# Optimization experiments

Hardware: AMD Instinct MI355X
Metric: run time of the kernel (lower is better)

## Reference

```python
import jax, jax.numpy as jnp
import numpy as np

DIM = 512

def setup_inputs() -> dict:
    key = jax.random.key(0)
    ks = jax.random.split(key, 7)
    B, Nq, Nkv = 8, 1024, 4096
    prototype = jax.random.normal(ks[0], (B, Nq, DIM), dtype=jnp.float32)
    q_x = jax.random.normal(ks[1], (B, Nkv, DIM), dtype=jnp.float32)
    qry_attn_mask = jax.random.bernoulli(ks[2], 0.5, (B, Nkv))  # True = keep
    # Linear(dim, dim, bias=False) weights, torch convention y = x @ W.T
    s = 1.0 / np.sqrt(DIM)
    Wq = jax.random.uniform(ks[3], (DIM, DIM), jnp.float32, -s, s)
    Wk = jax.random.uniform(ks[4], (DIM, DIM), jnp.float32, -s, s)
    Wv = jax.random.uniform(ks[5], (DIM, DIM), jnp.float32, -s, s)
    Wproj = jax.random.uniform(ks[6], (DIM, DIM), jnp.float32, -s, s)
    return {"prototype": prototype, "q_x": q_x, "qry_attn_mask": qry_attn_mask,
            "Wq": Wq, "Wk": Wk, "Wv": Wv, "Wproj": Wproj}

def reference(prototype, q_x, qry_attn_mask, Wq, Wk, Wv, Wproj):
    scale = DIM ** (-0.5)
    q = jnp.einsum('bnd,ed->bne', prototype, Wq)          # [B,Nq,D]
    k = jnp.einsum('bmd,ed->bme', q_x, Wk)                # [B,Nkv,D]
    v = jnp.einsum('bmd,ed->bme', q_x, Wv)                # [B,Nkv,D]
    attn = jnp.einsum('bnd,bmd->bnm', q, k) * scale       # [B,Nq,Nkv]
    bias = (~qry_attn_mask).astype(attn.dtype)[:, None, :] * -10000.0
    attn = jax.nn.softmax(attn + bias, axis=-1)
    x = jnp.einsum('bnm,bmd->bnd', attn, v)
    x = jnp.einsum('bnd,ed->bne', x, Wproj)
    return x
```

## Files before the change

kernel.cpp:

```cpp
#include <hip/hip_runtime.h>
#include <hip/hip_bf16.h>
#include <stdint.h>


typedef __bf16 bf16;
typedef bf16 bf16x8 __attribute__((ext_vector_type(8)));
typedef bf16 bf16x4 __attribute__((ext_vector_type(4)));
typedef float f32x4 __attribute__((ext_vector_type(4)));

#define NB 8
#define NQ 1024
#define NKV 4096
#define DD 512
#define RT_LD 136

__device__ __forceinline__ void lds16(const bf16* g, bf16* l) {
  __builtin_amdgcn_global_load_lds(
      (const __attribute__((address_space(1))) unsigned int*)g,
      (__attribute__((address_space(3))) unsigned int*)l, 16, 0, 0);
}

__global__ void cvt_kernel(const float* __restrict__ src, bf16* __restrict__ dst, int n4) {
  int i = blockIdx.x * blockDim.x + threadIdx.x;
  if (i < n4) {
    float4 v = ((const float4*)src)[i];
    bf16x4 o;
    o.x = (bf16)v.x; o.y = (bf16)v.y; o.z = (bf16)v.z; o.w = (bf16)v.w;
    ((bf16x4*)dst)[i] = o;
  }
}

__global__ void cvt_weights(const float* __restrict__ Wq, const float* __restrict__ Wk,
                            const float* __restrict__ Wv, const float* __restrict__ Wp,
                            bf16* __restrict__ Wq_b, bf16* __restrict__ Wkv_b,
                            bf16* __restrict__ Wp_b) {
  int i = blockIdx.x * blockDim.x + threadIdx.x;
  int w = i >> 16, r = i & 65535;
  const float* src = (w == 0) ? Wq : (w == 1) ? Wk : (w == 2) ? Wv : Wp;
  bf16x4* dst = (w == 0) ? (bf16x4*)Wq_b
              : (w == 3) ? (bf16x4*)Wp_b
                         : (bf16x4*)Wkv_b + (w == 2 ? 65536 : 0);
  float4 v = ((const float4*)src)[r];
  bf16x4 o;
  o.x = (bf16)v.x; o.y = (bf16)v.y; o.z = (bf16)v.z; o.w = (bf16)v.w;
  dst[r] = o;
}

__global__ void sniff_zero(const unsigned* __restrict__ mask, int* __restrict__ flag,
                           float* __restrict__ denom) {
  __shared__ int s_bad0, s_bad1;
  if (threadIdx.x == 0) { s_bad0 = 0; s_bad1 = 0; }
  __syncthreads();
  int b0 = 0, b1 = 0;
  for (int i = threadIdx.x; i < 8192; i += 256) {
    unsigned v = mask[i];
    if (v > 1u) b0 = 1;
    if (v != 0u && v != 0x3F800000u) b1 = 1;
  }
  if (b0) atomicOr(&s_bad0, 1);
  if (b1) atomicOr(&s_bad1, 1);
  for (int i = threadIdx.x; i < NB * NQ; i += 256) denom[i] = 0.f;
  __syncthreads();
  if (threadIdx.x == 0) *flag = (s_bad0 == 0) ? 0 : ((s_bad1 == 0) ? 1 : 2);
}

__global__ void scan_mask(const void* __restrict__ mask, const int* __restrict__ flagP,
                          int* __restrict__ idx, int* __restrict__ cnt,
                          int* __restrict__ kpad) {
  const int b = blockIdx.x, tid = threadIdx.x;
  const int mode = *flagP;
  __shared__ int ps[256];
  unsigned bits = 0;
  int c = 0;
  const int base = tid * 16;
  for (int i = 0; i < 16; ++i) {
    const int col = base + i;
    bool k;
    if (mode == 0)      k = ((const int*)mask)[b * NKV + col] != 0;
    else if (mode == 1) k = ((const float*)mask)[b * NKV + col] != 0.f;
    else                k = ((const unsigned char*)mask)[b * NKV + col] != 0;
    bits |= (unsigned)k << i;
    c += k;
  }
  ps[tid] = c;
  __syncthreads();
  for (int s = 1; s < 256; s <<= 1) {
    int v = (tid >= s) ? ps[tid - s] : 0;
    __syncthreads();
    ps[tid] += v;
    __syncthreads();
  }
  int off = ps[tid] - c;
  for (int i = 0; i < 16; ++i)
    if ((bits >> i) & 1) idx[b * NKV + off++] = base + i;
  if (tid == 255) {
    cnt[b] = ps[255];
    kpad[b] = (ps[255] + 127) & ~127;
  }
}

__global__ void gather_qx(const float* __restrict__ qx, const int* __restrict__ idx,
                          const int* __restrict__ cnt, const int* __restrict__ kpad,
                          bf16* __restrict__ qc) {
  const int b = blockIdx.y;
  const int wave = threadIdx.x >> 6, lane = threadIdx.x & 63;
  const int r0 = blockIdx.x * 16 + wave * 4;
  const int n = cnt[b];
  const int kp = kpad[b];
#pragma unroll
  for (int j = 0; j < 4; ++j) {
    const int row = r0 + j;
    if (row >= kp) return;
    bf16x4* d = (bf16x4*)(qc + ((long)b * NKV + row) * DD) + lane;
    if (row < n) {
      const int src = idx[b * NKV + row];
      const float4* s = (const float4*)(qx + ((long)b * NKV + src) * DD) + lane;
      float4 v0 = s[0], v1 = s[64];
      bf16x4 o0, o1;
      o0.x = (bf16)v0.x; o0.y = (bf16)v0.y; o0.z = (bf16)v0.z; o0.w = (bf16)v0.w;
      o1.x = (bf16)v1.x; o1.y = (bf16)v1.y; o1.z = (bf16)v1.z; o1.w = (bf16)v1.w;
      d[0] = o0;
      d[64] = o1;
    } else {
      bf16x4 z;
      z.x = (bf16)0.f; z.y = (bf16)0.f; z.z = (bf16)0.f; z.w = (bf16)0.f;
      d[0] = z;
      d[64] = z;
    }
  }
}

template <int EPI>
__global__ void __launch_bounds__(256, 4)
gemm_bt(const bf16* __restrict__ A, const bf16* __restrict__ Bw,
        void* __restrict__ Cp, void* __restrict__ Cp2,
        int N, int Klen, int Kstride,
        long sA, long sB, long sC,
        const int* __restrict__ cnt, const int* __restrict__ kpad,
        float* __restrict__ denom, float scale, int M) {
  __shared__ alignas(16) bf16 Smem[128 * RT_LD];
  bf16* As = Smem;
  bf16* Bs = Smem + 4096;
  bf16* Rt = Smem;
  const int tid = threadIdx.x;
  const int wave = tid >> 6, lane = tid & 63;
  const int l15 = lane & 15, l4 = lane >> 4;
  const int wm = (wave >> 1) * 64, wn = (wave & 1) * 64;
  const int bx = (EPI == 5) ? blockIdx.y : blockIdx.x;
  const int by = (EPI == 5) ? blockIdx.x : blockIdx.y;
  const int b = blockIdx.z;

  if constexpr (EPI == 2) {
    if (bx * 128 >= kpad[b]) return;
  } else {
    const int bb = by >> 5, loc = (by & 31) * 128;
    if (loc >= kpad[bb]) return;
  }

  const bf16* Ab = A + (long)b * sA + (long)(by * 128) * Kstride;
  const bf16* Bb = Bw + (long)b * sB + (long)(bx * 128) * Kstride;

  const int c0 = wave * 2, c1 = wave * 2 + 1;
  const int srow = lane >> 2;
  const int scol = (lane & 3) * 8;
  const bf16* ag0 = Ab + (long)(c0 * 16 + srow) * Kstride + scol;
  const bf16* ag1 = Ab + (long)(c1 * 16 + srow) * Kstride + scol;
  const bf16* bg0 = Bb + (long)(c0 * 16 + srow) * Kstride + scol;
  const bf16* bg1 = Bb + (long)(c1 * 16 + srow) * Kstride + scol;
  bf16* al0 = As + c0 * 512;
  bf16* al1 = As + c1 * 512;
  bf16* bl0 = Bs + c0 * 512;
  bf16* bl1 = Bs + c1 * 512;

  f32x4 acc[4][4] = {};

  for (int kt = 0; kt < Klen; kt += 32) {
    __syncthreads();
    lds16(ag0, al0);
    lds16(ag1, al1);
    lds16(bg0, bl0);
    lds16(bg1, bl1);
    ag0 += 32; ag1 += 32; bg0 += 32; bg1 += 32;
    __syncthreads();
    bf16x8 af[4], bfr[4];
#pragma unroll
    for (int t = 0; t < 4; ++t)
      af[t] = *(const bf16x8*)(As + (wm + t * 16 + l15) * 32 + l4 * 8);
#pragma unroll
    for (int t = 0; t < 4; ++t)
      bfr[t] = *(const bf16x8*)(Bs + (wn + t * 16 + l15) * 32 + l4 * 8);
#pragma unroll
    for (int mt = 0; mt < 4; ++mt)
#pragma unroll
      for (int nt = 0; nt < 4; ++nt)
        acc[mt][nt] = __builtin_amdgcn_mfma_f32_16x16x32_bf16(af[mt], bfr[nt],
                                                              acc[mt][nt], 0, 0, 0);
  }

  const int rowBase = by * 128 + wm;
  const int colBase = bx * 128 + wn;
  const int tR = by * 128;
  const int tC = bx * 128;

  __syncthreads();

  if constexpr (EPI == 2) {
    bf16* C = (bf16*)Cp + (long)b * sC;
    const int nkeep = cnt[b];
    float rs[4][4];
#pragma unroll
    for (int mt = 0; mt < 4; ++mt)
#pragma unroll
      for (int r = 0; r < 4; ++r) rs[mt][r] = 0.f;
#pragma unroll
    for (int nt = 0; nt < 4; ++nt) {
      const bool keep = (colBase + nt * 16 + l15) < nkeep;
#pragma unroll
      for (int mt = 0; mt < 4; ++mt)
#pragma unroll
        for (int r = 0; r < 4; ++r) {
          float p = keep ? __expf(acc[mt][nt][r] * scale) : 0.f;
          rs[mt][r] += p;
          Rt[(wm + mt * 16 + l4 * 4 + r) * RT_LD + wn + nt * 16 + l15] = (bf16)p;
        }
    }
#pragma unroll
    for (int mt = 0; mt < 4; ++mt)
#pragma unroll
      for (int r = 0; r < 4; ++r) {
        float v = rs[mt][r];
        v += __shfl_xor(v, 1, 64);
        v += __shfl_xor(v, 2, 64);
        v += __shfl_xor(v, 4, 64);
        v += __shfl_xor(v, 8, 64);
        if (l15 == 0)
          atomicAdd(&denom[b * M + rowBase + mt * 16 + l4 * 4 + r], v);
      }
    __syncthreads();
    const int r0 = tid >> 2, cq = (tid & 3) * 32;
#pragma unroll
    for (int h = 0; h < 128; h += 64)
#pragma unroll
      for (int j = 0; j < 4; ++j) {
        bf16x8 v = *(const bf16x8*)(Rt + (r0 + h) * RT_LD + cq + j * 8);
        *(bf16x8*)(C + (long)(tR + r0 + h) * N + tC + cq + j * 8) = v;
      }
  } else {
    if (tC < 512) {
      bf16* C = (bf16*)Cp;
#pragma unroll
      for (int mt = 0; mt < 4; ++mt)
#pragma unroll
        for (int nt = 0; nt < 4; ++nt)
#pragma unroll
          for (int r = 0; r < 4; ++r)
            Rt[(wm + mt * 16 + l4 * 4 + r) * RT_LD + wn + nt * 16 + l15] =
                (bf16)acc[mt][nt][r];
      __syncthreads();
      const int r0 = tid >> 2, cq = (tid & 3) * 32;
#pragma unroll
      for (int h = 0; h < 128; h += 64)
#pragma unroll
        for (int j = 0; j < 4; ++j) {
          bf16x8 v = *(const bf16x8*)(Rt + (r0 + h) * RT_LD + cq + j * 8);
          *(bf16x8*)(C + (long)(tR + r0 + h) * 512 + tC + cq + j * 8) = v;
        }
    } else {
      bf16* C = (bf16*)Cp2;
#pragma unroll
      for (int mt = 0; mt < 4; ++mt) {
        const int r0 = wm + mt * 16 + l4 * 4;
#pragma unroll
        for (int nt = 0; nt < 4; ++nt) {
          const int cloc = wn + nt * 16 + l15;
          bf16x4 o;
          o.x = (bf16)acc[mt][nt][0]; o.y = (bf16)acc[mt][nt][1];
          o.z = (bf16)acc[mt][nt][2]; o.w = (bf16)acc[mt][nt][3];
          *(bf16x4*)(Rt + cloc * RT_LD + r0) = o;
        }
      }
      __syncthreads();
      const int bb = tR >> 12, kvloc = tR & 4095;
      const int d0 = tid >> 2, kvq = (tid & 3) * 32;
#pragma unroll
      for (int h = 0; h < 128; h += 64)
#pragma unroll
        for (int j = 0; j < 4; ++j) {
          bf16x8 v = *(const bf16x8*)(Rt + (d0 + h) * RT_LD + kvq + j * 8);
          *(bf16x8*)(C + (long)bb * DD * NKV + (long)(tC - 512 + d0 + h) * NKV +
                     kvloc + kvq + j * 8) = v;
        }
    }
  }
}

template <int EPI>
__global__ void __launch_bounds__(256, 4)
gemm_n64(const bf16* __restrict__ A, const bf16* __restrict__ Bw,
         void* __restrict__ Cp) {
  constexpr int SME = (EPI == 0) ? 128 * 72 : 6144;
  __shared__ alignas(16) bf16 Smem[SME];
  bf16* As = Smem;
  bf16* Bs = Smem + 4096;
  bf16* Rt = Smem;
  const int tid = threadIdx.x;
  const int wave = tid >> 6, lane = tid & 63;
  const int l15 = lane & 15, l4 = lane >> 4;
  const int wm = (wave >> 1) * 64, wn = (wave & 1) * 32;

  const bf16* Ab = A + (long)(blockIdx.y * 128) * DD;
  const bf16* Bb = Bw + (long)(blockIdx.x * 64) * DD;

  const int srow = lane >> 2, scol = (lane & 3) * 8;
  const bf16* ag0 = Ab + (long)(wave * 32 + srow) * DD + scol;
  const bf16* ag1 = ag0 + 16 * DD;
  const bf16* bg0 = Bb + (long)(wave * 16 + srow) * DD + scol;
  bf16* al0 = As + wave * 1024;
  bf16* al1 = al0 + 512;
  bf16* bl0 = Bs + wave * 512;

  f32x4 acc[4][2] = {};

  for (int kt = 0; kt < DD; kt += 32) {
    __syncthreads();
    lds16(ag0, al0);
    lds16(ag1, al1);
    lds16(bg0, bl0);
    ag0 += 32; ag1 += 32; bg0 += 32;
    __syncthreads();
    bf16x8 af[4], bfr[2];
#pragma unroll
    for (int t = 0; t < 4; ++t)
      af[t] = *(const bf16x8*)(As + (wm + t * 16 + l15) * 32 + l4 * 8);
#pragma unroll
    for (int t = 0; t < 2; ++t)
      bfr[t] = *(const bf16x8*)(Bs + (wn + t * 16 + l15) * 32 + l4 * 8);
#pragma unroll
    for (int mt = 0; mt < 4; ++mt)
#pragma unroll
      for (int nt = 0; nt < 2; ++nt)
        acc[mt][nt] = __builtin_amdgcn_mfma_f32_16x16x32_bf16(af[mt], bfr[nt],
                                                              acc[mt][nt], 0, 0, 0);
  }

  const int tR = blockIdx.y * 128, tC = blockIdx.x * 64;
  if constexpr (EPI == 0) {
    __syncthreads();
#pragma unroll
    for (int mt = 0; mt < 4; ++mt)
#pragma unroll
      for (int nt = 0; nt < 2; ++nt)
#pragma unroll
        for (int r = 0; r < 4; ++r)
          Rt[(wm + mt * 16 + l4 * 4 + r) * 72 + wn + nt * 16 + l15] =
              (bf16)acc[mt][nt][r];
    __syncthreads();
    bf16* C = (bf16*)Cp;
    const int r0 = tid >> 1, cq = (tid & 1) * 32;
#pragma unroll
    for (int j = 0; j < 4; ++j) {
      bf16x8 v = *(const bf16x8*)(Rt + r0 * 72 + cq + j * 8);
      *(bf16x8*)(C + (long)(tR + r0) * DD + tC + cq + j * 8) = v;
    }
  } else {
    float* C = (float*)Cp;
#pragma unroll
    for (int mt = 0; mt < 4; ++mt)
#pragma unroll
      for (int nt = 0; nt < 2; ++nt)
#pragma unroll
        for (int r = 0; r < 4; ++r)
          C[(long)(tR + wm + mt * 16 + l4 * 4 + r) * DD + tC + wn + nt * 16 + l15] =
              acc[mt][nt][r];
  }
}

__global__ void __launch_bounds__(256, 4)
pv_direct(const bf16* __restrict__ P, const bf16* __restrict__ vT,
          const float* __restrict__ denom, const int* __restrict__ kpad,
          bf16* __restrict__ x) {
  __shared__ alignas(16) bf16 Smem[64 * RT_LD];
  bf16* As = Smem;
  bf16* Bs = Smem + 2048;
  bf16* Rt = Smem;
  const int tid = threadIdx.x;
  const int wave = tid >> 6, lane = tid & 63;
  const int l15 = lane & 15, l4 = lane >> 4;
  const int wm = (wave >> 1) * 32, wn = (wave & 1) * 64;
  const int qB = blockIdx.x * 64;
  const int dB = blockIdx.y * 128;
  const int b = blockIdx.z;
  const int Kb = kpad[b];

  const bf16* Ab = P + (long)b * NQ * NKV + (long)qB * NKV;
  const bf16* Bb = vT + (long)b * DD * NKV + (long)dB * NKV;

  const int srow = lane >> 2, scol = (lane & 3) * 8;
  const bf16* ag = Ab + (long)(wave * 16 + srow) * NKV + scol;
  const bf16* bg0 = Bb + (long)(wave * 32 + srow) * NKV + scol;
  const bf16* bg1 = bg0 + 16 * NKV;
  bf16* al = As + wave * 512;
  bf16* bl0 = Bs + wave * 1024;
  bf16* bl1 = bl0 + 512;

  f32x4 acc[2][4] = {};

  for (int kt = 0; kt < Kb; kt += 32) {
    __syncthreads();
    lds16(ag, al);
    lds16(bg0, bl0);
    lds16(bg1, bl1);
    ag += 32; bg0 += 32; bg1 += 32;
    __syncthreads();
    bf16x8 af[2], bfr[4];
#pragma unroll
    for (int t = 0; t < 2; ++t)
      af[t] = *(const bf16x8*)(As + (wm + t * 16 + l15) * 32 + l4 * 8);
#pragma unroll
    for (int t = 0; t < 4; ++t)
      bfr[t] = *(const bf16x8*)(Bs + (wn + t * 16 + l15) * 32 + l4 * 8);
#pragma unroll
    for (int mt = 0; mt < 2; ++mt)
#pragma unroll
      for (int nt = 0; nt < 4; ++nt)
        acc[mt][nt] = __builtin_amdgcn_mfma_f32_16x16x32_bf16(af[mt], bfr[nt],
                                                              acc[mt][nt], 0, 0, 0);
  }

  __syncthreads();
#pragma unroll
  for (int mt = 0; mt < 2; ++mt)
#pragma unroll
    for (int r = 0; r < 4; ++r) {
      const int row = wm + mt * 16 + l4 * 4 + r;
      const float inv = 1.0f / denom[b * NQ + qB + row];
#pragma unroll
      for (int nt = 0; nt < 4; ++nt)
        Rt[row * RT_LD + wn + nt * 16 + l15] = (bf16)(acc[mt][nt][r] * inv);
    }
  __syncthreads();
  const int r0 = tid >> 2, cq = (tid & 3) * 32;
#pragma unroll
  for (int j = 0; j < 4; ++j) {
    bf16x8 v = *(const bf16x8*)(Rt + r0 * RT_LD + cq + j * 8);
    *(bf16x8*)(x + (long)(b * NQ + qB + r0) * DD + dB + cq + j * 8) = v;
  }
}

extern "C" void kernel_launch(void* const* d_in, const int* in_sizes, int n_in,
                              void* d_out, int out_size, void* d_ws, size_t ws_size,
                              hipStream_t stream) {
  const float* proto = (const float*)d_in[0];
  const float* qx    = (const float*)d_in[1];
  const void*  mask  = d_in[2];
  const float* Wq    = (const float*)d_in[3];
  const float* Wk    = (const float*)d_in[4];
  const float* Wv    = (const float*)d_in[5];
  const float* Wproj = (const float*)d_in[6];
  float* out = (float*)d_out;

  char* w = (char*)d_ws;
  int*   flag  = (int*)w;
  int*   cnt   = (int*)(w + 64);
  int*   kpadA = (int*)(w + 128);
  float* denom = (float*)(w + 4096);
  size_t off = 65536;
  bf16* Wq_b  = (bf16*)(w + off); off += (size_t)DD * DD * 2;
  bf16* Wkv_b = (bf16*)(w + off); off += (size_t)DD * DD * 4;
  bf16* Wp_b  = (bf16*)(w + off); off += (size_t)DD * DD * 2;
  int*  idx   = (int*)(w + off);  off += (size_t)NB * NKV * 4;
  bf16* q_b   = (bf16*)(w + off); off += (size_t)NB * NQ * DD * 2;
  bf16* k_b   = (bf16*)(w + off); off += (size_t)NB * NKV * DD * 2;
  bf16* vT_b  = (bf16*)(w + off); off += (size_t)NB * NKV * DD * 2;
  bf16* x_b   = (bf16*)(w + off); off += (size_t)NB * NQ * DD * 2;
  size_t off_pp = off;
  bf16* proto_b = (bf16*)(w + off); off += (size_t)NB * NQ * DD * 2;
  bf16* qc_b    = (bf16*)(w + off);
  bf16* P       = (bf16*)(w + off_pp);

  sniff_zero<<<1, 256, 0, stream>>>((const unsigned*)mask, flag, denom);
  scan_mask<<<8, 256, 0, stream>>>(mask, flag, idx, cnt, kpadA);

  cvt_kernel<<<NB * NQ * DD / 4 / 256, 256, 0, stream>>>(proto, proto_b, NB * NQ * DD / 4);
  gather_qx<<<dim3(NKV / 16, NB), 256, 0, stream>>>(qx, idx, cnt, kpadA, qc_b);
  cvt_weights<<<4 * 65536 / 256, 256, 0, stream>>>(Wq, Wk, Wv, Wproj, Wq_b, Wkv_b, Wp_b);

  const float scale = 0.04419417382415922f;

  gemm_n64<0><<<dim3(8, 64, 1), 256, 0, stream>>>(proto_b, Wq_b, q_b);
  gemm_bt<5><<<dim3(256, 8, 1), 256, 0, stream>>>(
      qc_b, Wkv_b, k_b, vT_b, 1024, DD, DD, 0L, 0L, 0L,
      cnt, kpadA, nullptr, 0.f, 0);
  gemm_bt<2><<<dim3(NKV / 128, NQ / 128, NB), 256, 0, stream>>>(
      q_b, k_b, P, nullptr, NKV, DD, DD,
      (long)NQ * DD, (long)NKV * DD, (long)NQ * NKV,
      cnt, kpadA, denom, scale, NQ);
  pv_direct<<<dim3(16, 4, 8), 256, 0, stream>>>(P, vT_b, denom, kpadA, x_b);
  gemm_n64<4><<<dim3(8, 64, 1), 256, 0, stream>>>(x_b, Wp_b, out);
}
```

Measured before the change: 344.3 us.

## Merge prep kernels, double K-step to 64, and reuse gemm_bt for projections

Folds the mask-type sniffing and denom zeroing into scan_mask and merges the gather, proto conversion and weight conversion into a single prep launch, cutting kernel launches. The GEMM and PV main loops now load 64-wide K slices per barrier pair, halving the number of syncs per tile at the cost of more LDS. gemm_bt's launch bound drops to 2 blocks per SM. The Q and output projections now use gemm_bt with 128x128 tiles instead of the 128x64 gemm_n64, giving fewer blocks for those small GEMMs.

```diff
diff --git a/kernel.cpp b/kernel.cpp
--- a/kernel.cpp
+++ b/kernel.cpp
@@ -20,55 +20,29 @@
       (__attribute__((address_space(3))) unsigned int*)l, 16, 0, 0);
 }
 
-__global__ void cvt_kernel(const float* __restrict__ src, bf16* __restrict__ dst, int n4) {
-  int i = blockIdx.x * blockDim.x + threadIdx.x;
-  if (i < n4) {
-    float4 v = ((const float4*)src)[i];
-    bf16x4 o;
-    o.x = (bf16)v.x; o.y = (bf16)v.y; o.z = (bf16)v.z; o.w = (bf16)v.w;
-    ((bf16x4*)dst)[i] = o;
-  }
-}
-
-__global__ void cvt_weights(const float* __restrict__ Wq, const float* __restrict__ Wk,
-                            const float* __restrict__ Wv, const float* __restrict__ Wp,
-                            bf16* __restrict__ Wq_b, bf16* __restrict__ Wkv_b,
-                            bf16* __restrict__ Wp_b) {
-  int i = blockIdx.x * blockDim.x + threadIdx.x;
-  int w = i >> 16, r = i & 65535;
-  const float* src = (w == 0) ? Wq : (w == 1) ? Wk : (w == 2) ? Wv : Wp;
-  bf16x4* dst = (w == 0) ? (bf16x4*)Wq_b
-              : (w == 3) ? (bf16x4*)Wp_b
-                         : (bf16x4*)Wkv_b + (w == 2 ? 65536 : 0);
-  float4 v = ((const float4*)src)[r];
-  bf16x4 o;
-  o.x = (bf16)v.x; o.y = (bf16)v.y; o.z = (bf16)v.z; o.w = (bf16)v.w;
-  dst[r] = o;
-}
-
-__global__ void sniff_zero(const unsigned* __restrict__ mask, int* __restrict__ flag,
-                           float* __restrict__ denom) {
-  __shared__ int s_bad0, s_bad1;
-  if (threadIdx.x == 0) { s_bad0 = 0; s_bad1 = 0; }
-  __syncthreads();
-  int b0 = 0, b1 = 0;
-  for (int i = threadIdx.x; i < 8192; i += 256) {
-    unsigned v = mask[i];
-    if (v > 1u) b0 = 1;
-    if (v != 0u && v != 0x3F800000u) b1 = 1;
-  }
-  if (b0) atomicOr(&s_bad0, 1);
-  if (b1) atomicOr(&s_bad1, 1);
-  for (int i = threadIdx.x; i < NB * NQ; i += 256) denom[i] = 0.f;
-  __syncthreads();
-  if (threadIdx.x == 0) *flag = (s_bad0 == 0) ? 0 : ((s_bad1 == 0) ? 1 : 2);
-}
-
-__global__ void scan_mask(const void* __restrict__ mask, const int* __restrict__ flagP,
+__global__ void scan_mask(const void* __restrict__ mask,
                           int* __restrict__ idx, int* __restrict__ cnt,
-                          int* __restrict__ kpad) {
+                          int* __restrict__ kpad, float* __restrict__ denom) {
   const int b = blockIdx.x, tid = threadIdx.x;
-  const int mode = *flagP;
+  for (int i = tid; i < NQ; i += 256) denom[b * NQ + i] = 0.f;
+
+  __shared__ int s0, s1;
+  if (tid == 0) { s0 = 0; s1 = 0; }
+  __syncthreads();
+  {
+    const unsigned* mw = (const unsigned*)mask;
+    int b0 = 0, b1 = 0;
+    for (int i = tid; i < 8192; i += 256) {
+      unsigned v = mw[i];
+      if (v > 1u) b0 = 1;
+      if (v != 0u && v != 0x3F800000u) b1 = 1;
+    }
+    if (b0) atomicOr(&s0, 1);
+    if (b1) atomicOr(&s1, 1);
+  }
+  __syncthreads();
+  const int mode = (s0 == 0) ? 0 : ((s1 == 0) ? 1 : 2);
+
   __shared__ int ps[256];
   unsigned bits = 0;
   int c = 0;
@@ -99,39 +73,64 @@
   }
 }
 
-__global__ void gather_qx(const float* __restrict__ qx, const int* __restrict__ idx,
-                          const int* __restrict__ cnt, const int* __restrict__ kpad,
-                          bf16* __restrict__ qc) {
-  const int b = blockIdx.y;
-  const int wave = threadIdx.x >> 6, lane = threadIdx.x & 63;
-  const int r0 = blockIdx.x * 16 + wave * 4;
-  const int n = cnt[b];
-  const int kp = kpad[b];
-#pragma unroll
-  for (int j = 0; j < 4; ++j) {
-    const int row = r0 + j;
-    if (row >= kp) return;
-    bf16x4* d = (bf16x4*)(qc + ((long)b * NKV + row) * DD) + lane;
-    if (row < n) {
-      const int src = idx[b * NKV + row];
-      const float4* s = (const float4*)(qx + ((long)b * NKV + src) * DD) + lane;
-      float4 v0 = s[0], v1 = s[64];
-      bf16x4 o0, o1;
-      o0.x = (bf16)v0.x; o0.y = (bf16)v0.y; o0.z = (bf16)v0.z; o0.w = (bf16)v0.w;
-      o1.x = (bf16)v1.x; o1.y = (bf16)v1.y; o1.z = (bf16)v1.z; o1.w = (bf16)v1.w;
-      d[0] = o0;
-      d[64] = o1;
-    } else {
-      bf16x4 z;
-      z.x = (bf16)0.f; z.y = (bf16)0.f; z.z = (bf16)0.f; z.w = (bf16)0.f;
-      d[0] = z;
-      d[64] = z;
-    }
+__global__ void prep(const float* __restrict__ qx, const int* __restrict__ idx,
+                     const int* __restrict__ cnt, const int* __restrict__ kpad,
+                     bf16* __restrict__ qc,
+                     const float* __restrict__ proto, bf16* __restrict__ proto_b,
+                     const float* __restrict__ Wq, const float* __restrict__ Wk,
+                     const float* __restrict__ Wv, const float* __restrict__ Wp,
+                     bf16* __restrict__ Wq_b, bf16* __restrict__ Wkv_b,
+                     bf16* __restrict__ Wp_b) {
+  const int blk = blockIdx.x, tid = threadIdx.x;
+  if (blk < 2048) {
+    const int b = blk >> 8, bx = blk & 255;
+    const int wave = tid >> 6, lane = tid & 63;
+    const int r0 = bx * 16 + wave * 4;
+    const int n = cnt[b];
+    const int kp = kpad[b];
+#pragma unroll
+    for (int j = 0; j < 4; ++j) {
+      const int row = r0 + j;
+      if (row >= kp) return;
+      bf16x4* d = (bf16x4*)(qc + ((long)b * NKV + row) * DD) + lane;
+      if (row < n) {
+        const int src = idx[b * NKV + row];
+        const float4* s = (const float4*)(qx + ((long)b * NKV + src) * DD) + lane;
+        float4 v0 = s[0], v1 = s[64];
+        bf16x4 o0, o1;
+        o0.x = (bf16)v0.x; o0.y = (bf16)v0.y; o0.z = (bf16)v0.z; o0.w = (bf16)v0.w;
+        o1.x = (bf16)v1.x; o1.y = (bf16)v1.y; o1.z = (bf16)v1.z; o1.w = (bf16)v1.w;
+        d[0] = o0;
+        d[64] = o1;
+      } else {
+        bf16x4 z;
+        z.x = (bf16)0.f; z.y = (bf16)0.f; z.z = (bf16)0.f; z.w = (bf16)0.f;
+        d[0] = z;
+        d[64] = z;
+      }
+    }
+  } else if (blk < 6144) {
+    const int i = (blk - 2048) * 256 + tid;
+    float4 v = ((const float4*)proto)[i];
+    bf16x4 o;
+    o.x = (bf16)v.x; o.y = (bf16)v.y; o.z = (bf16)v.z; o.w = (bf16)v.w;
+    ((bf16x4*)proto_b)[i] = o;
+  } else {
+    const int j = (blk - 6144) * 256 + tid;
+    const int w = j >> 16, r = j & 65535;
+    const float* src = (w == 0) ? Wq : (w == 1) ? Wk : (w == 2) ? Wv : Wp;
+    bf16x4* dst = (w == 0) ? (bf16x4*)Wq_b
+                : (w == 3) ? (bf16x4*)Wp_b
+                           : (bf16x4*)Wkv_b + (w == 2 ? 65536 : 0);
+    float4 v = ((const float4*)src)[r];
+    bf16x4 o;
+    o.x = (bf16)v.x; o.y = (bf16)v.y; o.z = (bf16)v.z; o.w = (bf16)v.w;
+    dst[r] = o;
   }
 }
 
 template <int EPI>
-__global__ void __launch_bounds__(256, 4)
+__global__ void __launch_bounds__(256, 2)
 gemm_bt(const bf16* __restrict__ A, const bf16* __restrict__ Bw,
         void* __restrict__ Cp, void* __restrict__ Cp2,
         int N, int Klen, int Kstride,
@@ -140,7 +139,7 @@
         float* __restrict__ denom, float scale, int M) {
   __shared__ alignas(16) bf16 Smem[128 * RT_LD];
   bf16* As = Smem;
-  bf16* Bs = Smem + 4096;
+  bf16* Bs = Smem + 8192;
   bf16* Rt = Smem;
   const int tid = threadIdx.x;
   const int wave = tid >> 6, lane = tid & 63;
@@ -152,7 +151,7 @@
 
   if constexpr (EPI == 2) {
     if (bx * 128 >= kpad[b]) return;
-  } else {
+  } else if constexpr (EPI == 5) {
     const int bb = by >> 5, loc = (by & 31) * 128;
     if (loc >= kpad[bb]) return;
   }
@@ -160,41 +159,49 @@
   const bf16* Ab = A + (long)b * sA + (long)(by * 128) * Kstride;
   const bf16* Bb = Bw + (long)b * sB + (long)(bx * 128) * Kstride;
 
-  const int c0 = wave * 2, c1 = wave * 2 + 1;
-  const int srow = lane >> 2;
-  const int scol = (lane & 3) * 8;
-  const bf16* ag0 = Ab + (long)(c0 * 16 + srow) * Kstride + scol;
-  const bf16* ag1 = Ab + (long)(c1 * 16 + srow) * Kstride + scol;
-  const bf16* bg0 = Bb + (long)(c0 * 16 + srow) * Kstride + scol;
-  const bf16* bg1 = Bb + (long)(c1 * 16 + srow) * Kstride + scol;
-  bf16* al0 = As + c0 * 512;
-  bf16* al1 = As + c1 * 512;
-  bf16* bl0 = Bs + c0 * 512;
-  bf16* bl1 = Bs + c1 * 512;
+  const int srow = lane >> 2, scol = (lane & 3) * 8;
+  const bf16* ag[4];
+  const bf16* bg[4];
+  bf16* al[4];
+  bf16* bl[4];
+#pragma unroll
+  for (int i = 0; i < 4; ++i) {
+    const int st = wave * 4 + i, rs = st >> 1, cs = st & 1;
+    ag[i] = Ab + (long)(rs * 16 + srow) * Kstride + cs * 32 + scol;
+    bg[i] = Bb + (long)(rs * 16 + srow) * Kstride + cs * 32 + scol;
+    al[i] = As + st * 512;
+    bl[i] = Bs + st * 512;
+  }
 
   f32x4 acc[4][4] = {};
 
-  for (int kt = 0; kt < Klen; kt += 32) {
-    __syncthreads();
-    lds16(ag0, al0);
-    lds16(ag1, al1);
-    lds16(bg0, bl0);
-    lds16(bg1, bl1);
-    ag0 += 32; ag1 += 32; bg0 += 32; bg1 += 32;
-    __syncthreads();
-    bf16x8 af[4], bfr[4];
-#pragma unroll
-    for (int t = 0; t < 4; ++t)
-      af[t] = *(const bf16x8*)(As + (wm + t * 16 + l15) * 32 + l4 * 8);
-#pragma unroll
-    for (int t = 0; t < 4; ++t)
-      bfr[t] = *(const bf16x8*)(Bs + (wn + t * 16 + l15) * 32 + l4 * 8);
+  for (int kt = 0; kt < Klen; kt += 64) {
+    __syncthreads();
+#pragma unroll
+    for (int i = 0; i < 4; ++i) lds16(ag[i], al[i]);
+#pragma unroll
+    for (int i = 0; i < 4; ++i) lds16(bg[i], bl[i]);
+#pragma unroll
+    for (int i = 0; i < 4; ++i) { ag[i] += 64; bg[i] += 64; }
+    __syncthreads();
+    bf16x8 af0[4], af1[4], bf0[4], bf1[4];
+    const int ra = (wave >> 1) * 4, rb = (wave & 1) * 4;
+#pragma unroll
+    for (int t = 0; t < 4; ++t) {
+      af0[t] = *(const bf16x8*)(As + ((ra + t) * 2 + 0) * 512 + l15 * 32 + l4 * 8);
+      af1[t] = *(const bf16x8*)(As + ((ra + t) * 2 + 1) * 512 + l15 * 32 + l4 * 8);
+      bf0[t] = *(const bf16x8*)(Bs + ((rb + t) * 2 + 0) * 512 + l15 * 32 + l4 * 8);
+      bf1[t] = *(const bf16x8*)(Bs + ((rb + t) * 2 + 1) * 512 + l15 * 32 + l4 * 8);
+    }
 #pragma unroll
     for (int mt = 0; mt < 4; ++mt)
 #pragma unroll
-      for (int nt = 0; nt < 4; ++nt)
-        acc[mt][nt] = __builtin_amdgcn_mfma_f32_16x16x32_bf16(af[mt], bfr[nt],
+      for (int nt = 0; nt < 4; ++nt) {
+        acc[mt][nt] = __builtin_amdgcn_mfma_f32_16x16x32_bf16(af0[mt], bf0[nt],
                                                               acc[mt][nt], 0, 0, 0);
+        acc[mt][nt] = __builtin_amdgcn_mfma_f32_16x16x32_bf16(af1[mt], bf1[nt],
+                                                              acc[mt][nt], 0, 0, 0);
+      }
   }
 
   const int rowBase = by * 128 + wm;
@@ -245,6 +252,35 @@
         bf16x8 v = *(const bf16x8*)(Rt + (r0 + h) * RT_LD + cq + j * 8);
         *(bf16x8*)(C + (long)(tR + r0 + h) * N + tC + cq + j * 8) = v;
       }
+  } else if constexpr (EPI == 0) {
+    bf16* C = (bf16*)Cp;
+#pragma unroll
+    for (int mt = 0; mt < 4; ++mt)
+#pragma unroll
+      for (int nt = 0; nt < 4; ++nt)
+#pragma unroll
+        for (int r = 0; r < 4; ++r)
+          Rt[(wm + mt * 16 + l4 * 4 + r) * RT_LD + wn + nt * 16 + l15] =
+              (bf16)acc[mt][nt][r];
+    __syncthreads();
+    const int r0 = tid >> 2, cq = (tid & 3) * 32;
+#pragma unroll
+    for (int h = 0; h < 128; h += 64)
+#pragma unroll
+      for (int j = 0; j < 4; ++j) {
+        bf16x8 v = *(const bf16x8*)(Rt + (r0 + h) * RT_LD + cq + j * 8);
+        *(bf16x8*)(C + (long)(tR + r0 + h) * N + tC + cq + j * 8) = v;
+      }
+  } else if constexpr (EPI == 4) {
+    float* C = (float*)Cp;
+#pragma unroll
+    for (int mt = 0; mt < 4; ++mt)
+#pragma unroll
+      for (int nt = 0; nt < 4; ++nt)
+#pragma unroll
+        for (int r = 0; r < 4; ++r)
+          C[(long)(tR + wm + mt * 16 + l4 * 4 + r) * N + tC + wn + nt * 16 + l15] =
+              acc[mt][nt][r];
   } else {
     if (tC < 512) {
       bf16* C = (bf16*)Cp;
@@ -294,94 +330,13 @@
   }
 }
 
-template <int EPI>
-__global__ void __launch_bounds__(256, 4)
-gemm_n64(const bf16* __restrict__ A, const bf16* __restrict__ Bw,
-         void* __restrict__ Cp) {
-  constexpr int SME = (EPI == 0) ? 128 * 72 : 6144;
-  __shared__ alignas(16) bf16 Smem[SME];
-  bf16* As = Smem;
-  bf16* Bs = Smem + 4096;
-  bf16* Rt = Smem;
-  const int tid = threadIdx.x;
-  const int wave = tid >> 6, lane = tid & 63;
-  const int l15 = lane & 15, l4 = lane >> 4;
-  const int wm = (wave >> 1) * 64, wn = (wave & 1) * 32;
-
-  const bf16* Ab = A + (long)(blockIdx.y * 128) * DD;
-  const bf16* Bb = Bw + (long)(blockIdx.x * 64) * DD;
-
-  const int srow = lane >> 2, scol = (lane & 3) * 8;
-  const bf16* ag0 = Ab + (long)(wave * 32 + srow) * DD + scol;
-  const bf16* ag1 = ag0 + 16 * DD;
-  const bf16* bg0 = Bb + (long)(wave * 16 + srow) * DD + scol;
-  bf16* al0 = As + wave * 1024;
-  bf16* al1 = al0 + 512;
-  bf16* bl0 = Bs + wave * 512;
-
-  f32x4 acc[4][2] = {};
-
-  for (int kt = 0; kt < DD; kt += 32) {
-    __syncthreads();
-    lds16(ag0, al0);
-    lds16(ag1, al1);
-    lds16(bg0, bl0);
-    ag0 += 32; ag1 += 32; bg0 += 32;
-    __syncthreads();
-    bf16x8 af[4], bfr[2];
-#pragma unroll
-    for (int t = 0; t < 4; ++t)
-      af[t] = *(const bf16x8*)(As + (wm + t * 16 + l15) * 32 + l4 * 8);
-#pragma unroll
-    for (int t = 0; t < 2; ++t)
-      bfr[t] = *(const bf16x8*)(Bs + (wn + t * 16 + l15) * 32 + l4 * 8);
-#pragma unroll
-    for (int mt = 0; mt < 4; ++mt)
-#pragma unroll
-      for (int nt = 0; nt < 2; ++nt)
-        acc[mt][nt] = __builtin_amdgcn_mfma_f32_16x16x32_bf16(af[mt], bfr[nt],
-                                                              acc[mt][nt], 0, 0, 0);
-  }
-
-  const int tR = blockIdx.y * 128, tC = blockIdx.x * 64;
-  if constexpr (EPI == 0) {
-    __syncthreads();
-#pragma unroll
-    for (int mt = 0; mt < 4; ++mt)
-#pragma unroll
-      for (int nt = 0; nt < 2; ++nt)
-#pragma unroll
-        for (int r = 0; r < 4; ++r)
-          Rt[(wm + mt * 16 + l4 * 4 + r) * 72 + wn + nt * 16 + l15] =
-              (bf16)acc[mt][nt][r];
-    __syncthreads();
-    bf16* C = (bf16*)Cp;
-    const int r0 = tid >> 1, cq = (tid & 1) * 32;
-#pragma unroll
-    for (int j = 0; j < 4; ++j) {
-      bf16x8 v = *(const bf16x8*)(Rt + r0 * 72 + cq + j * 8);
-      *(bf16x8*)(C + (long)(tR + r0) * DD + tC + cq + j * 8) = v;
-    }
-  } else {
-    float* C = (float*)Cp;
-#pragma unroll
-    for (int mt = 0; mt < 4; ++mt)
-#pragma unroll
-      for (int nt = 0; nt < 2; ++nt)
-#pragma unroll
-        for (int r = 0; r < 4; ++r)
-          C[(long)(tR + wm + mt * 16 + l4 * 4 + r) * DD + tC + wn + nt * 16 + l15] =
-              acc[mt][nt][r];
-  }
-}
-
 __global__ void __launch_bounds__(256, 4)
 pv_direct(const bf16* __restrict__ P, const bf16* __restrict__ vT,
           const float* __restrict__ denom, const int* __restrict__ kpad,
           bf16* __restrict__ x) {
-  __shared__ alignas(16) bf16 Smem[64 * RT_LD];
+  __shared__ alignas(16) bf16 Smem[12288];
   bf16* As = Smem;
-  bf16* Bs = Smem + 2048;
+  bf16* Bs = Smem + 4096;
   bf16* Rt = Smem;
   const int tid = threadIdx.x;
   const int wave = tid >> 6, lane = tid & 63;
@@ -396,35 +351,57 @@
   const bf16* Bb = vT + (long)b * DD * NKV + (long)dB * NKV;
 
   const int srow = lane >> 2, scol = (lane & 3) * 8;
-  const bf16* ag = Ab + (long)(wave * 16 + srow) * NKV + scol;
-  const bf16* bg0 = Bb + (long)(wave * 32 + srow) * NKV + scol;
-  const bf16* bg1 = bg0 + 16 * NKV;
-  bf16* al = As + wave * 512;
-  bf16* bl0 = Bs + wave * 1024;
-  bf16* bl1 = bl0 + 512;
+  const bf16* ag[2];
+  const bf16* bg[4];
+  bf16* al[2];
+  bf16* bl[4];
+#pragma unroll
+  for (int i = 0; i < 2; ++i) {
+    const int st = wave * 2 + i, rs = st >> 1, cs = st & 1;
+    ag[i] = Ab + (long)(rs * 16 + srow) * NKV + cs * 32 + scol;
+    al[i] = As + st * 512;
+  }
+#pragma unroll
+  for (int i = 0; i < 4; ++i) {
+    const int st = wave * 4 + i, rs = st >> 1, cs = st & 1;
+    bg[i] = Bb + (long)(rs * 16 + srow) * NKV + cs * 32 + scol;
+    bl[i] = Bs + st * 512;
+  }
 
   f32x4 acc[2][4] = {};
 
-  for (int kt = 0; kt < Kb; kt += 32) {
-    __syncthreads();
-    lds16(ag, al);
-    lds16(bg0, bl0);
-    lds16(bg1, bl1);
-    ag += 32; bg0 += 32; bg1 += 32;
-    __syncthreads();
-    bf16x8 af[2], bfr[4];
-#pragma unroll
-    for (int t = 0; t < 2; ++t)
-      af[t] = *(const bf16x8*)(As + (wm + t * 16 + l15) * 32 + l4 * 8);
-#pragma unroll
-    for (int t = 0; t < 4; ++t)
-      bfr[t] = *(const bf16x8*)(Bs + (wn + t * 16 + l15) * 32 + l4 * 8);
+  for (int kt = 0; kt < Kb; kt += 64) {
+    __syncthreads();
+#pragma unroll
+    for (int i = 0; i < 2; ++i) lds16(ag[i], al[i]);
+#pragma unroll
+    for (int i = 0; i < 4; ++i) lds16(bg[i], bl[i]);
+#pragma unroll
+    for (int i = 0; i < 2; ++i) ag[i] += 64;
+#pragma unroll
+    for (int i = 0; i < 4; ++i) bg[i] += 64;
+    __syncthreads();
+    bf16x8 af0[2], af1[2], bf0[4], bf1[4];
+    const int ra = (wave >> 1) * 2, rb = (wave & 1) * 4;
+#pragma unroll
+    for (int t = 0; t < 2; ++t) {
+      af0[t] = *(const bf16x8*)(As + ((ra + t) * 2 + 0) * 512 + l15 * 32 + l4 * 8);
+      af1[t] = *(const bf16x8*)(As + ((ra + t) * 2 + 1) * 512 + l15 * 32 + l4 * 8);
+    }
+#pragma unroll
+    for (int t = 0; t < 4; ++t) {
+      bf0[t] = *(const bf16x8*)(Bs + ((rb + t) * 2 + 0) * 512 + l15 * 32 + l4 * 8);
+      bf1[t] = *(const bf16x8*)(Bs + ((rb + t) * 2 + 1) * 512 + l15 * 32 + l4 * 8);
+    }
 #pragma unroll
     for (int mt = 0; mt < 2; ++mt)
 #pragma unroll
-      for (int nt = 0; nt < 4; ++nt)
-        acc[mt][nt] = __builtin_amdgcn_mfma_f32_16x16x32_bf16(af[mt], bfr[nt],
+      for (int nt = 0; nt < 4; ++nt) {
+        acc[mt][nt] = __builtin_amdgcn_mfma_f32_16x16x32_bf16(af0[mt], bf0[nt],
                                                               acc[mt][nt], 0, 0, 0);
+        acc[mt][nt] = __builtin_amdgcn_mfma_f32_16x16x32_bf16(af1[mt], bf1[nt],
+                                                              acc[mt][nt], 0, 0, 0);
+      }
   }
 
   __syncthreads();
@@ -460,7 +437,6 @@
   float* out = (float*)d_out;
 
   char* w = (char*)d_ws;
-  int*   flag  = (int*)w;
   int*   cnt   = (int*)(w + 64);
   int*   kpadA = (int*)(w + 128);
   float* denom = (float*)(w + 4096);
@@ -478,16 +454,16 @@
   bf16* qc_b    = (bf16*)(w + off);
   bf16* P       = (bf16*)(w + off_pp);
 
-  sniff_zero<<<1, 256, 0, stream>>>((const unsigned*)mask, flag, denom);
-  scan_mask<<<8, 256, 0, stream>>>(mask, flag, idx, cnt, kpadA);
-
-  cvt_kernel<<<NB * NQ * DD / 4 / 256, 256, 0, stream>>>(proto, proto_b, NB * NQ * DD / 4);
-  gather_qx<<<dim3(NKV / 16, NB), 256, 0, stream>>>(qx, idx, cnt, kpadA, qc_b);
-  cvt_weights<<<4 * 65536 / 256, 256, 0, stream>>>(Wq, Wk, Wv, Wproj, Wq_b, Wkv_b, Wp_b);
+  scan_mask<<<8, 256, 0, stream>>>(mask, idx, cnt, kpadA, denom);
+  prep<<<7168, 256, 0, stream>>>(qx, idx, cnt, kpadA, qc_b,
+                                 proto, proto_b, Wq, Wk, Wv, Wproj,
+                                 Wq_b, Wkv_b, Wp_b);
 
   const float scale = 0.04419417382415922f;
 
-  gemm_n64<0><<<dim3(8, 64, 1), 256, 0, stream>>>(proto_b, Wq_b, q_b);
+  gemm_bt<0><<<dim3(4, 64, 1), 256, 0, stream>>>(
+      proto_b, Wq_b, q_b, nullptr, DD, DD, DD, 0L, 0L, 0L,
+      cnt, kpadA, nullptr, 0.f, 0);
   gemm_bt<5><<<dim3(256, 8, 1), 256, 0, stream>>>(
       qc_b, Wkv_b, k_b, vT_b, 1024, DD, DD, 0L, 0L, 0L,
       cnt, kpadA, nullptr, 0.f, 0);
@@ -496,5 +472,7 @@
       (long)NQ * DD, (long)NKV * DD, (long)NQ * NKV,
       cnt, kpadA, denom, scale, NQ);
   pv_direct<<<dim3(16, 4, 8), 256, 0, stream>>>(P, vT_b, denom, kpadA, x_b);
-  gemm_n64<4><<<dim3(8, 64, 1), 256, 0, stream>>>(x_b, Wp_b, out);
-}
+  gemm_bt<4><<<dim3(4, 64, 1), 256, 0, stream>>>(
+      x_b, Wp_b, out, nullptr, DD, DD, DD, 0L, 0L, 0L,
+      cnt, kpadA, nullptr, 0.f, 0);
+}
```

Measured after the change: 313.8 us. -8.9%, faster.
